# Optimization experiments

Measured on AMD Instinct MI355X. Metric: run time of the kernel, lower is better.

The kernel has to match this reference:

```python
import jax, jax.numpy as jnp
import numpy as np

# dims
B, TQ, NQ, DQ = 2, 32, 196, 896      # batch, chunks, queries/chunk, slow-feat dim
T, H, W, CIN = 32, 8, 8, 4           # fast feature video dims
EMB = 1024                           # fast input mapping (kv) dim
HID = 512                            # cross_attn_hidden_dim
NH = 4                               # heads
HD = HID // NH                       # head dim = 128
HALF = HD // 2                       # 64 rotary freq channels
SEC = [22, 21, 21]                   # 3D rope sections (t,h,w) over the 64 freqs
FF = 2 * HID
OUT = 896
BASE = 10000.0
QGRID = 14                           # 196 = 14x14 query spatial grid
EPS = 1e-5


def _p(key, shape, scale=0.02):
    return (jax.random.normal(key, shape, dtype=jnp.float32) * scale)


def setup_inputs() -> dict:
    key = jax.random.key(0)
    ks = jax.random.split(key, 20)
    inp = {
        "x": jax.random.normal(ks[0], (B, T, H, W, CIN), dtype=jnp.float32),
        "slow_feats": jax.random.normal(ks[1], (B, TQ, NQ, DQ), dtype=jnp.float32),
        "frame_num": jnp.full((B,), T, dtype=jnp.int32),
        # query_input_mapping: 896 -> 512
        "Wq_in": _p(ks[2], (DQ, HID)), "bq_in": jnp.zeros((HID,), jnp.float32),
        # fast input_mapping (linear): 4 -> 1024
        "Wm": _p(ks[3], (CIN, EMB)), "bm": jnp.zeros((EMB,), jnp.float32),
        # cross-attn projections
        "Wq": _p(ks[4], (HID, HID)), "bq": jnp.zeros((HID,), jnp.float32),
        "Wk": _p(ks[5], (EMB, HID)), "bk": jnp.zeros((HID,), jnp.float32),
        "Wv": _p(ks[6], (EMB, HID)), "bv": jnp.zeros((HID,), jnp.float32),
        "Wo": _p(ks[7], (HID, HID)), "bo": jnp.zeros((HID,), jnp.float32),
        # decoder layer norms + FFN (dim_feedforward = 2*hidden)
        "g1": jnp.ones((HID,), jnp.float32), "be1": jnp.zeros((HID,), jnp.float32),
        "W1": _p(ks[8], (HID, FF)), "b1": jnp.zeros((FF,), jnp.float32),
        "W2": _p(ks[9], (FF, HID)), "b2": jnp.zeros((HID,), jnp.float32),
        "g2": jnp.ones((HID,), jnp.float32), "be2": jnp.zeros((HID,), jnp.float32),
        # output MLP (mlp_depth=2): 512 -> 1024 -> GELU -> 896
        "M1": _p(ks[10], (HID, 2 * HID)), "bm1": jnp.zeros((2 * HID,), jnp.float32),
        "M2": _p(ks[11], (2 * HID, OUT)), "bm2": jnp.zeros((OUT,), jnp.float32),
    }
    return inp


def _ln(x, g, b):
    m = x.mean(-1, keepdims=True)
    v = jnp.var(x, axis=-1, keepdims=True)
    return (x - m) * jax.lax.rsqrt(v + EPS) * g + b


def _rope_cos_sin(pos):
    # pos: (N,3) float (t,h,w). Qwen2-style inv_freq over head_dim=128.
    inv_freq = 1.0 / (BASE ** (jnp.arange(0, HD, 2, dtype=jnp.float32) / HD))  # (64,)
    sel = jnp.asarray([0] * SEC[0] + [1] * SEC[1] + [2] * SEC[2])              # (64,)
    freqs = pos[:, sel] * inv_freq                                             # (N,64)
    emb = jnp.concatenate([freqs, freqs], axis=-1)                             # (N,128)
    return jnp.cos(emb), jnp.sin(emb)


def _rot_half(x):
    return jnp.concatenate([-x[..., HALF:], x[..., :HALF]], axis=-1)


def _positions():
    # query tokens: (chunk t, 14x14 grid)
    qt = jnp.repeat(jnp.arange(TQ), NQ)
    qg = jnp.tile(jnp.arange(NQ), TQ)
    q_pos = jnp.stack([qt, qg // QGRID, qg % QGRID], axis=-1).astype(jnp.float32)  # (6272,3)
    # kv tokens: (frame t, HxW grid)
    kt = jnp.repeat(jnp.arange(T), H * W)
    kg = jnp.tile(jnp.arange(H * W), T)
    k_pos = jnp.stack([kt, kg // W, kg % W], axis=-1).astype(jnp.float32)          # (2048,3)
    return q_pos, k_pos


def _forward(x, slow_feats, Wq_in, bq_in, Wm, bm, Wq, bq, Wk, bk, Wv, bv,
             Wo, bo, g1, be1, W1, b1, W2, b2, g2, be2, M1, bm1, M2, bm2):
    q_pos, k_pos = _positions()
    cos_q, sin_q = _rope_cos_sin(q_pos)   # (Nq,128)
    cos_k, sin_k = _rope_cos_sin(k_pos)   # (Nk,128)
    scale = 1.0 / jnp.sqrt(jnp.float32(HD))

    def per_sample(xi, si):
        # slow feats -> queries: (32,196,896) -> (6272,512)
        q_in = (si.reshape(TQ * NQ, DQ) @ Wq_in + bq_in)
        # fast feats -> kv tokens: (T,H,W,Cin) -> (2048,1024)
        kv = (xi.reshape(T * H * W, CIN) @ Wm + bm)
        # projections -> heads
        q = (q_in @ Wq + bq).reshape(-1, NH, HD)
        k = (kv @ Wk + bk).reshape(-1, NH, HD)
        v = (kv @ Wv + bv).reshape(-1, NH, HD)
        # 3D RoPE on q and k
        q = q * cos_q[:, None, :] + _rot_half(q) * sin_q[:, None, :]
        k = k * cos_k[:, None, :] + _rot_half(k) * sin_k[:, None, :]
        # cross attention
        attn = jnp.einsum('qhd,khd->hqk', q, k) * scale
        attn = jax.nn.softmax(attn, axis=-1)
        o = jnp.einsum('hqk,khd->qhd', attn, v).reshape(-1, HID)
        o = o @ Wo + bo
        # residual + norm + FFN + norm (post-norm decoder layer)
        h = _ln(q_in + o, g1, be1)
        ff = jax.nn.gelu(h @ W1 + b1) @ W2 + b2
        h = _ln(h + ff, g2, be2)
        # output MLP: Linear -> GELU -> Linear
        y = jax.nn.gelu(h @ M1 + bm1) @ M2 + bm2
        return y  # (6272, 896)

    return jax.vmap(per_sample)(x, slow_feats)  # (B, 6272, 896)


def reference(x, slow_feats, frame_num, Wq_in, bq_in, Wm, bm, Wq, bq, Wk, bk,
              Wv, bv, Wo, bo, g1, be1, W1, b1, W2, b2, g2, be2, M1, bm1, M2, bm2):
    # frame_num is the valid-frame count per sample; here all samples are full
    # length (frame_num == T), so no KV masking is needed.
    del frame_num
    return _forward(x, slow_feats, Wq_in, bq_in, Wm, bm, Wq, bq, Wk, bk, Wv, bv,
                    Wo, bo, g1, be1, W1, b1, W2, b2, g2, be2, M1, bm1, M2, bm2)
```

## Files before the change

kernel.cpp:

```cpp
#include <hip/hip_runtime.h>
#include <cstdint>
#include <cstddef>

#define BATCH 2
#define MQ 12544
#define ROWS_Q 6272
#define MK 4096
#define ROWS_K 2048
#define HID 512
#define NH 4
#define HD 128
#define EMB 1024
#define DQ 896
#define FF 1024
#define OUTD 896

typedef __bf16 bf16;
typedef unsigned int u32;
typedef bf16 bf16x8 __attribute__((ext_vector_type(8)));
typedef bf16 bf16x4 __attribute__((ext_vector_type(4)));
typedef float f32x4 __attribute__((ext_vector_type(4)));

enum { OP_BIAS = 0, OP_GELU = 1, OP_RES = 2 };

__device__ __forceinline__ float gelu_tanh(float x) {
    float x3 = x * x * x;
    return 0.5f * x * (1.0f + tanhf(0.7978845608028654f * (x + 0.044715f * x3)));
}

__device__ __forceinline__ void gld16(const bf16* g, bf16* l) {
    __builtin_amdgcn_global_load_lds(
        (const __attribute__((address_space(1))) unsigned int*)g,
        (__attribute__((address_space(3))) unsigned int*)l, 16, 0, 0);
}

__device__ __forceinline__ u32 pack_bf16(float a, float b) {
    union { bf16 h[2]; u32 w; } u;
    u.h[0] = (bf16)a; u.h[1] = (bf16)b;
    return u.w;
}

template <int OP, bool WF32, bool WB16>
__global__ __launch_bounds__(256) void mgemm(
    const bf16* __restrict__ A, const bf16* __restrict__ Bt,
    const float* __restrict__ bias, const float* __restrict__ res,
    float* __restrict__ Cf, bf16* __restrict__ Cb, int M, int N, int K)
{
    __shared__ __align__(16) bf16 As0[128 * 32];
    __shared__ __align__(16) bf16 As1[128 * 32];
    __shared__ __align__(16) bf16 Bs0[128 * 32];
    __shared__ __align__(16) bf16 Bs1[128 * 32];
    const int tid  = threadIdx.x;
    const int m0   = blockIdx.y * 128;
    const int n0   = blockIdx.x * 128;
    const int wave = tid >> 6, lane = tid & 63;
    const int wm = (wave >> 1) * 64, wn = (wave & 1) * 64;

    f32x4 acc[4][4] = {};

    const int srow = tid >> 2;
    const int scol = (tid & 3) * 8;
    const bf16* Ag = A  + (size_t)(m0 + srow) * K + scol;
    const bf16* Bg = Bt + (size_t)(n0 + srow) * K + scol;
    bf16* Al0 = &As0[tid * 8];
    bf16* Al1 = &As1[tid * 8];
    bf16* Bl0 = &Bs0[tid * 8];
    bf16* Bl1 = &Bs1[tid * 8];
    const size_t half = (size_t)64 * K;

    const int fr = lane & 15;
    const int kq = (lane >> 4) * 8;
    const bf16* pa0 = &As0[(wm + fr) * 32 + kq];
    const bf16* pa1 = &As1[(wm + fr) * 32 + kq];
    const bf16* pb0 = &Bs0[(wn + fr) * 32 + kq];
    const bf16* pb1 = &Bs1[(wn + fr) * 32 + kq];

    gld16(Ag,        Al0);
    gld16(Ag + half, Al0 + 64 * 32);
    gld16(Bg,        Bl0);
    gld16(Bg + half, Bl0 + 64 * 32);

    for (int k0 = 0; k0 < K; k0 += 64) {
        __syncthreads();
        gld16(Ag + k0 + 32,        Al1);
        gld16(Ag + k0 + 32 + half, Al1 + 64 * 32);
        gld16(Bg + k0 + 32,        Bl1);
        gld16(Bg + k0 + 32 + half, Bl1 + 64 * 32);
        {
            bf16x8 af[4], bfr[4];
            #pragma unroll
            for (int i = 0; i < 4; ++i) af[i]  = *(const bf16x8*)(pa0 + i * 16 * 32);
            #pragma unroll
            for (int j = 0; j < 4; ++j) bfr[j] = *(const bf16x8*)(pb0 + j * 16 * 32);
            #pragma unroll
            for (int i = 0; i < 4; ++i)
                #pragma unroll
                for (int j = 0; j < 4; ++j)
                    acc[i][j] = __builtin_amdgcn_mfma_f32_16x16x32_bf16(
                        af[i], bfr[j], acc[i][j], 0, 0, 0);
        }
        __syncthreads();
        if (k0 + 64 < K) {
            gld16(Ag + k0 + 64,        Al0);
            gld16(Ag + k0 + 64 + half, Al0 + 64 * 32);
            gld16(Bg + k0 + 64,        Bl0);
            gld16(Bg + k0 + 64 + half, Bl0 + 64 * 32);
        }
        {
            bf16x8 af[4], bfr[4];
            #pragma unroll
            for (int i = 0; i < 4; ++i) af[i]  = *(const bf16x8*)(pa1 + i * 16 * 32);
            #pragma unroll
            for (int j = 0; j < 4; ++j) bfr[j] = *(const bf16x8*)(pb1 + j * 16 * 32);
            #pragma unroll
            for (int i = 0; i < 4; ++i)
                #pragma unroll
                for (int j = 0; j < 4; ++j)
                    acc[i][j] = __builtin_amdgcn_mfma_f32_16x16x32_bf16(
                        af[i], bfr[j], acc[i][j], 0, 0, 0);
        }
    }

    const int colb = n0 + wn + (lane & 15);
    const int rowb = m0 + wm + (lane >> 4) * 4;
    #pragma unroll
    for (int i = 0; i < 4; ++i) {
        #pragma unroll
        for (int j = 0; j < 4; ++j) {
            const int c = colb + j * 16;
            const float bj = bias[c];
            #pragma unroll
            for (int r = 0; r < 4; ++r) {
                const int m = rowb + i * 16 + r;
                float v = acc[i][j][r] + bj;
                if (OP == OP_GELU) v = gelu_tanh(v);
                if (OP == OP_RES)  v += res[(size_t)m * N + c];
                if (WF32) Cf[(size_t)m * N + c] = v;
                if (WB16) Cb[(size_t)m * N + c] = (bf16)v;
            }
        }
    }
}

template <int OP, bool WF32, bool WB16>
__global__ __launch_bounds__(256) void mgemm64(
    const bf16* __restrict__ A, const bf16* __restrict__ Bt,
    const float* __restrict__ bias, const float* __restrict__ res,
    float* __restrict__ Cf, bf16* __restrict__ Cb, int M, int N, int K)
{
    __shared__ __align__(16) bf16 As0[64 * 32];
    __shared__ __align__(16) bf16 As1[64 * 32];
    __shared__ __align__(16) bf16 Bs0[128 * 32];
    __shared__ __align__(16) bf16 Bs1[128 * 32];
    const int tid  = threadIdx.x;
    const int m0   = blockIdx.y * 64;
    const int n0   = blockIdx.x * 128;
    const int wave = tid >> 6, lane = tid & 63;
    const int wm = (wave >> 1) * 32, wn = (wave & 1) * 64;

    f32x4 acc[2][4] = {};

    const int srow = tid >> 2;
    const int scol = (tid & 3) * 8;
    const bf16* Ag = A  + (size_t)(m0 + srow) * K + scol;
    const bf16* Bg = Bt + (size_t)(n0 + srow) * K + scol;
    bf16* Al0 = &As0[tid * 8];
    bf16* Al1 = &As1[tid * 8];
    bf16* Bl0 = &Bs0[tid * 8];
    bf16* Bl1 = &Bs1[tid * 8];
    const size_t half = (size_t)64 * K;

    const int fr = lane & 15;
    const int kq = (lane >> 4) * 8;
    const bf16* pa0 = &As0[(wm + fr) * 32 + kq];
    const bf16* pa1 = &As1[(wm + fr) * 32 + kq];
    const bf16* pb0 = &Bs0[(wn + fr) * 32 + kq];
    const bf16* pb1 = &Bs1[(wn + fr) * 32 + kq];

    gld16(Ag,        Al0);
    gld16(Bg,        Bl0);
    gld16(Bg + half, Bl0 + 64 * 32);

    for (int k0 = 0; k0 < K; k0 += 64) {
        __syncthreads();
        gld16(Ag + k0 + 32,        Al1);
        gld16(Bg + k0 + 32,        Bl1);
        gld16(Bg + k0 + 32 + half, Bl1 + 64 * 32);
        {
            bf16x8 af[2], bfr[4];
            #pragma unroll
            for (int i = 0; i < 2; ++i) af[i]  = *(const bf16x8*)(pa0 + i * 16 * 32);
            #pragma unroll
            for (int j = 0; j < 4; ++j) bfr[j] = *(const bf16x8*)(pb0 + j * 16 * 32);
            #pragma unroll
            for (int i = 0; i < 2; ++i)
                #pragma unroll
                for (int j = 0; j < 4; ++j)
                    acc[i][j] = __builtin_amdgcn_mfma_f32_16x16x32_bf16(
                        af[i], bfr[j], acc[i][j], 0, 0, 0);
        }
        __syncthreads();
        if (k0 + 64 < K) {
            gld16(Ag + k0 + 64,        Al0);
            gld16(Bg + k0 + 64,        Bl0);
            gld16(Bg + k0 + 64 + half, Bl0 + 64 * 32);
        }
        {
            bf16x8 af[2], bfr[4];
            #pragma unroll
            for (int i = 0; i < 2; ++i) af[i]  = *(const bf16x8*)(pa1 + i * 16 * 32);
            #pragma unroll
            for (int j = 0; j < 4; ++j) bfr[j] = *(const bf16x8*)(pb1 + j * 16 * 32);
            #pragma unroll
            for (int i = 0; i < 2; ++i)
                #pragma unroll
                for (int j = 0; j < 4; ++j)
                    acc[i][j] = __builtin_amdgcn_mfma_f32_16x16x32_bf16(
                        af[i], bfr[j], acc[i][j], 0, 0, 0);
        }
    }

    const int colb = n0 + wn + (lane & 15);
    const int rowb = m0 + wm + (lane >> 4) * 4;
    #pragma unroll
    for (int i = 0; i < 2; ++i) {
        #pragma unroll
        for (int j = 0; j < 4; ++j) {
            const int c = colb + j * 16;
            const float bj = bias[c];
            #pragma unroll
            for (int r = 0; r < 4; ++r) {
                const int m = rowb + i * 16 + r;
                float v = acc[i][j][r] + bj;
                if (OP == OP_GELU) v = gelu_tanh(v);
                if (OP == OP_RES)  v += res[(size_t)m * N + c];
                if (WF32) Cf[(size_t)m * N + c] = v;
                if (WB16) Cb[(size_t)m * N + c] = (bf16)v;
            }
        }
    }
}

struct TDesc { const float* src; bf16* dst; int K; int N; int tile0; };
struct TDescs { TDesc d[9]; };

__global__ __launch_bounds__(256) void transpose_all(TDescs td)
{
    __shared__ float t[32][33];
    const int blk = blockIdx.x;
    int i = 0;
    #pragma unroll
    for (int j = 1; j < 9; ++j) if (blk >= td.d[j].tile0) i = j;
    const float* src = td.d[i].src;
    bf16* dst = td.d[i].dst;
    const int K = td.d[i].K, N = td.d[i].N;
    const int local = blk - td.d[i].tile0;
    const int ntx = N >> 5;
    const int bx = local % ntx, by = local / ntx;
    const int x = threadIdx.x & 31, y = threadIdx.x >> 5;
    #pragma unroll
    for (int p = 0; p < 32; p += 8)
        t[y + p][x] = src[(size_t)(by * 32 + y + p) * N + bx * 32 + x];
    __syncthreads();
    #pragma unroll
    for (int p = 0; p < 32; p += 8)
        dst[(size_t)(bx * 32 + y + p) * K + by * 32 + x] = (bf16)t[x][y + p];
}

__global__ __launch_bounds__(256) void cvt_kernel(
    const float* __restrict__ in, bf16* __restrict__ out, int n4)
{
    int i = blockIdx.x * 256 + threadIdx.x;
    if (i >= n4) return;
    float4 v = ((const float4*)in)[i];
    out[4 * i + 0] = (bf16)v.x;
    out[4 * i + 1] = (bf16)v.y;
    out[4 * i + 2] = (bf16)v.z;
    out[4 * i + 3] = (bf16)v.w;
}

__global__ __launch_bounds__(256) void kv_kernel(
    const float* __restrict__ x, const float* __restrict__ Wm,
    const float* __restrict__ bm, bf16* __restrict__ kv)
{
    int idx = blockIdx.x * 256 + threadIdx.x;
    int r = idx >> 10, n = idx & 1023;
    float4 xv = *(const float4*)(x + (size_t)r * 4);
    float v = bm[n] + xv.x * Wm[n] + xv.y * Wm[1024 + n]
                    + xv.z * Wm[2048 + n] + xv.w * Wm[3072 + n];
    kv[idx] = (bf16)v;
}

__global__ __launch_bounds__(256) void rope_tab_kernel(float2* __restrict__ tab)
{
    int i = blockIdx.x * 256 + threadIdx.x;
    if (i >= 64 * 32) return;
    int f = i >> 5, pos = i & 31;
    float ang = (float)pos * exp2f(-(float)f * 0.20762050593045954f);
    tab[i] = make_float2(cosf(ang), sinf(ang));
}

__global__ __launch_bounds__(256) void rope_b_kernel(
    const bf16* __restrict__ in, bf16* __restrict__ out,
    const float2* __restrict__ tab,
    int tok, int gdiv, int wdiv, int total, float sc, int istr, int icoff)
{
    int idx = blockIdx.x * 256 + threadIdx.x;
    if (idx >= total) return;
    int row = idx >> 7;
    int r2 = idx & 127;
    int h = r2 >> 5;
    int j2 = r2 & 31;
    int j = 2 * j2;
    int n = row % tok;
    int t = n / gdiv;
    int g = n % gdiv;
    int gh = g / wdiv;
    int gw = g % wdiv;
    int j1 = j + 1;
    int pa_i = (j < 22)  ? t : (j < 43)  ? gh : gw;
    int pb_i = (j1 < 22) ? t : (j1 < 43) ? gh : gw;
    float2 ta = tab[j * 32 + pa_i];
    float2 tb = tab[j1 * 32 + pb_i];
    float ca = ta.x, sa = ta.y;
    float cb = tb.x, sb = tb.y;
    size_t ibase = (size_t)row * istr + icoff + (size_t)h * 128 + j;
    size_t obase = (size_t)row * 512 + (size_t)h * 128 + j;
    union { u32 w; bf16 e[2]; } ua, ub;
    ua.w = *(const u32*)(in + ibase);
    ub.w = *(const u32*)(in + ibase + 64);
    float x1a = (float)ua.e[0], x1b = (float)ua.e[1];
    float x2a = (float)ub.e[0], x2b = (float)ub.e[1];
    *(u32*)(out + obase)      = pack_bf16((x1a * ca - x2a * sa) * sc,
                                          (x1b * cb - x2b * sb) * sc);
    *(u32*)(out + obase + 64) = pack_bf16((x2a * ca + x1a * sa) * sc,
                                          (x2b * cb + x1b * sb) * sc);
}

__global__ __launch_bounds__(256) void vt_tiled(
    const bf16* __restrict__ kv16, bf16* __restrict__ vt)
{
    __shared__ bf16 t[64][72];
    const int tt = blockIdx.x * 64;
    const int d0 = blockIdx.y * 64;
    const int bh = blockIdx.z;
    const int b = bh >> 2, h = bh & 3;
    const int rr = threadIdx.x >> 4;
    const int cc = (threadIdx.x & 15) * 4;
    #pragma unroll
    for (int p = 0; p < 4; ++p) {
        int r = rr + p * 16;
        *(bf16x4*)&t[r][cc] = *(const bf16x4*)
            (kv16 + (size_t)(b * ROWS_K + tt + r) * 1024 + 512 + h * 128 + d0 + cc);
    }
    __syncthreads();
    #pragma unroll
    for (int p = 0; p < 4; ++p) {
        int r = rr + p * 16;
        bf16x4 v;
        v[0] = t[cc + 0][r]; v[1] = t[cc + 1][r];
        v[2] = t[cc + 2][r]; v[3] = t[cc + 3][r];
        *(bf16x4*)(vt + (size_t)bh * HD * ROWS_K + (size_t)(d0 + r) * ROWS_K + tt + cc) = v;
    }
}

__global__ __launch_bounds__(256) void ln_kernel(
    float* __restrict__ xb, const float* __restrict__ g,
    const float* __restrict__ be, bf16* __restrict__ out16)
{
    int wave = threadIdx.x >> 6, lane = threadIdx.x & 63;
    size_t row = (size_t)blockIdx.x * 4 + wave;
    float* xp = xb + row * 512;
    float4 a = ((const float4*)xp)[lane];
    float4 b = ((const float4*)xp)[lane + 64];
    float s  = a.x + a.y + a.z + a.w + b.x + b.y + b.z + b.w;
    float sq = a.x*a.x + a.y*a.y + a.z*a.z + a.w*a.w
             + b.x*b.x + b.y*b.y + b.z*b.z + b.w*b.w;
    #pragma unroll
    for (int off = 32; off; off >>= 1) {
        s  += __shfl_xor(s, off);
        sq += __shfl_xor(sq, off);
    }
    float mean = s * (1.0f / 512.0f);
    float var  = sq * (1.0f / 512.0f) - mean * mean;
    float rstd = rsqrtf(var + 1e-5f);
    float4 gv1 = ((const float4*)g)[lane],  gv2 = ((const float4*)g)[lane + 64];
    float4 bv1 = ((const float4*)be)[lane], bv2 = ((const float4*)be)[lane + 64];
    a.x = (a.x - mean) * rstd * gv1.x + bv1.x;
    a.y = (a.y - mean) * rstd * gv1.y + bv1.y;
    a.z = (a.z - mean) * rstd * gv1.z + bv1.z;
    a.w = (a.w - mean) * rstd * gv1.w + bv1.w;
    b.x = (b.x - mean) * rstd * gv2.x + bv2.x;
    b.y = (b.y - mean) * rstd * gv2.y + bv2.y;
    b.z = (b.z - mean) * rstd * gv2.z + bv2.z;
    b.w = (b.w - mean) * rstd * gv2.w + bv2.w;
    ((float4*)xp)[lane]      = a;
    ((float4*)xp)[lane + 64] = b;
    bf16* op = out16 + row * 512;
    *(u32*)(op + lane * 4)       = pack_bf16(a.x, a.y);
    *(u32*)(op + lane * 4 + 2)   = pack_bf16(a.z, a.w);
    *(u32*)(op + 256 + lane * 4)     = pack_bf16(b.x, b.y);
    *(u32*)(op + 256 + lane * 4 + 2) = pack_bf16(b.z, b.w);
}

__global__ __launch_bounds__(256, 2) void mattn_kernel(
    const bf16* __restrict__ qs, const bf16* __restrict__ ks,
    const bf16* __restrict__ vt, bf16* __restrict__ outb)
{
    __shared__ __align__(16) char smem[35840];
    bf16* Ksh = (bf16*)smem;
    bf16* Vsh = (bf16*)(smem + 17408);

    const int tid = threadIdx.x;
    const int wave = tid >> 6, lane = tid & 63;
    const int quad = lane >> 4, c = lane & 15;
    const int bid = blockIdx.x;
    const int bh = bid & 7;
    const int qt = bid >> 3;
    const int h  = bh & 3;
    const int b  = bh >> 2;

    const int q0 = qt * 128 + wave * 32;
    const bf16* qg = qs + (size_t)(b * ROWS_Q + q0) * HID + h * HD;
    const bf16* kg = ks + (size_t)(b * ROWS_K) * HID + h * HD;
    const bf16* vg = vt + (size_t)(b * NH + h) * HD * ROWS_K;

    bf16x8 qf[2][4];
    #pragma unroll
    for (int n = 0; n < 2; ++n)
        #pragma unroll
        for (int s = 0; s < 4; ++s)
            qf[n][s] = *(const bf16x8*)(qg + (size_t)(n * 16 + c) * HID + s * 32 + quad * 8);

    f32x4 o[8][2] = {};
    float m_i[2] = {-1e30f, -1e30f}, l_i[2] = {0.0f, 0.0f};

    const int st_t = tid >> 2;
    const int st_d = (tid & 3) * 32;
    const int sv_d = tid >> 1;
    const int sv_t = (tid & 1) * 32;

    for (int kt = 0; kt < 32; ++kt) {
        __syncthreads();
        {
            const bf16* src = kg + (size_t)(kt * 64 + st_t) * HID + st_d;
            bf16* dst = Ksh + st_t * 136 + st_d;
            #pragma unroll
            for (int i = 0; i < 4; ++i)
                *(bf16x8*)(dst + i * 8) = *(const bf16x8*)(src + i * 8);
        }
        {
            const bf16* src = vg + (size_t)sv_d * ROWS_K + kt * 64 + sv_t;
            bf16* dst = Vsh + sv_d * 72 + sv_t;
            #pragma unroll
            for (int i = 0; i < 4; ++i)
                *(bf16x8*)(dst + i * 8) = *(const bf16x8*)(src + i * 8);
        }
        __syncthreads();

        f32x4 s[4][2] = {};
        #pragma unroll
        for (int ksi = 0; ksi < 4; ++ksi) {
            bf16x8 kf[4];
            #pragma unroll
            for (int mi = 0; mi < 4; ++mi)
                kf[mi] = *(const bf16x8*)(Ksh + (mi * 16 + c) * 136 + ksi * 32 + quad * 8);
            #pragma unroll
            for (int mi = 0; mi < 4; ++mi)
                #pragma unroll
                for (int n = 0; n < 2; ++n)
                    s[mi][n] = __builtin_amdgcn_mfma_f32_16x16x32_bf16(
                        kf[mi], qf[n][ksi], s[mi][n], 0, 0, 0);
        }

        float alpha[2];
        #pragma unroll
        for (int n = 0; n < 2; ++n) {
            float mx = -1e30f;
            #pragma unroll
            for (int mi = 0; mi < 4; ++mi)
                #pragma unroll
                for (int r = 0; r < 4; ++r) mx = fmaxf(mx, s[mi][n][r]);
            mx = fmaxf(mx, __shfl_xor(mx, 16));
            mx = fmaxf(mx, __shfl_xor(mx, 32));
            float mn = fmaxf(m_i[n], mx);
            alpha[n] = __expf(m_i[n] - mn);
            m_i[n] = mn;
            float sm = 0.0f;
            #pragma unroll
            for (int mi = 0; mi < 4; ++mi)
                #pragma unroll
                for (int r = 0; r < 4; ++r) {
                    float p = __expf(s[mi][n][r] - mn);
                    s[mi][n][r] = p;
                    sm += p;
                }
            sm += __shfl_xor(sm, 16);
            sm += __shfl_xor(sm, 32);
            l_i[n] = l_i[n] * alpha[n] + sm;
            #pragma unroll
            for (int md = 0; md < 8; ++md) {
                o[md][n][0] *= alpha[n]; o[md][n][1] *= alpha[n];
                o[md][n][2] *= alpha[n]; o[md][n][3] *= alpha[n];
            }
        }

        u32 pk[4][2][2];
        #pragma unroll
        for (int mi = 0; mi < 4; ++mi)
            #pragma unroll
            for (int n = 0; n < 2; ++n) {
                pk[mi][n][0] = pack_bf16(s[mi][n][0], s[mi][n][1]);
                pk[mi][n][1] = pack_bf16(s[mi][n][2], s[mi][n][3]);
            }
        bf16x8 pf[2][2];
        #pragma unroll
        for (int kst = 0; kst < 2; ++kst)
            #pragma unroll
            for (int n = 0; n < 2; ++n) {
                union { bf16x8 v8; u32 d[4]; } u;
                #pragma unroll
                for (int dw = 0; dw < 4; ++dw) {
                    int srcl = ((quad & 1) * 2 + (dw >> 1)) * 16 + c;
                    u32 lo = (u32)__shfl((int)pk[2 * kst][n][dw & 1], srcl);
                    u32 hi = (u32)__shfl((int)pk[2 * kst + 1][n][dw & 1], srcl);
                    u.d[dw] = (quad >= 2) ? hi : lo;
                }
                pf[kst][n] = u.v8;
            }

        #pragma unroll
        for (int kst = 0; kst < 2; ++kst)
            #pragma unroll
            for (int md = 0; md < 8; ++md) {
                bf16x8 vf = *(const bf16x8*)(Vsh + (md * 16 + c) * 72 + kst * 32 + quad * 8);
                #pragma unroll
                for (int n = 0; n < 2; ++n)
                    o[md][n] = __builtin_amdgcn_mfma_f32_16x16x32_bf16(
                        vf, pf[kst][n], o[md][n], 0, 0, 0);
            }
    }

    __syncthreads();
    bf16* Osh = (bf16*)smem + wave * (32 * 136);
    float inv[2] = {1.0f / l_i[0], 1.0f / l_i[1]};
    #pragma unroll
    for (int md = 0; md < 8; ++md)
        #pragma unroll
        for (int n = 0; n < 2; ++n)
            #pragma unroll
            for (int hh = 0; hh < 2; ++hh) {
                u32 w = pack_bf16(o[md][n][2 * hh] * inv[n], o[md][n][2 * hh + 1] * inv[n]);
                int d = md * 16 + quad * 4 + 2 * hh;
                int qq = n * 16 + c;
                *(u32*)(Osh + qq * 136 + d) = w;
            }
    __syncthreads();
    bf16* og = outb + (size_t)(b * ROWS_Q + q0) * HID + h * HD;
    #pragma unroll
    for (int i = 0; i < 8; ++i) {
        int idx = i * 64 + lane;
        int qq = idx >> 4;
        int ch = idx & 15;
        bf16x8 vv = *(const bf16x8*)(Osh + qq * 136 + ch * 8);
        *(bf16x8*)(og + (size_t)qq * HID + ch * 8) = vv;
    }
}

extern "C" void kernel_launch(void* const* d_in, const int* in_sizes, int n_in,
                              void* d_out, int out_size, void* d_ws, size_t ws_size,
                              hipStream_t stream)
{
    const float* x     = (const float*)d_in[0];
    const float* slow  = (const float*)d_in[1];
    const float* Wq_in = (const float*)d_in[3];
    const float* bq_in = (const float*)d_in[4];
    const float* Wm    = (const float*)d_in[5];
    const float* bm    = (const float*)d_in[6];
    const float* Wq    = (const float*)d_in[7];
    const float* bq    = (const float*)d_in[8];
    const float* Wk    = (const float*)d_in[9];
    const float* bk    = (const float*)d_in[10];
    const float* Wv    = (const float*)d_in[11];
    const float* bv    = (const float*)d_in[12];
    const float* Wo    = (const float*)d_in[13];
    const float* bo    = (const float*)d_in[14];
    const float* g1    = (const float*)d_in[15];
    const float* be1   = (const float*)d_in[16];
    const float* W1    = (const float*)d_in[17];
    const float* b1    = (const float*)d_in[18];
    const float* W2    = (const float*)d_in[19];
    const float* b2    = (const float*)d_in[20];
    const float* g2    = (const float*)d_in[21];
    const float* be2   = (const float*)d_in[22];
    const float* M1    = (const float*)d_in[23];
    const float* bm1   = (const float*)d_in[24];
    const float* M2    = (const float*)d_in[25];
    const float* bm2   = (const float*)d_in[26];
    float* out = (float*)d_out;

    float* q_in_f = (float*)d_ws;
    float* ob     = q_in_f + (size_t)MQ * HID;
    float* bkv    = ob + (size_t)MQ * HID;
    bf16* shared_b = (bf16*)(bkv + 1024);
    bf16* q_in_b = shared_b + (size_t)MQ * FF;
    bf16* kv_b   = q_in_b + (size_t)MQ * HID;
    bf16* h_b    = kv_b + (size_t)MK * EMB;
    bf16* q16    = h_b + (size_t)MQ * HID;
    bf16* kv16   = q16 + (size_t)MQ * HID;
    bf16* qbt    = kv16 + (size_t)MK * EMB;
    bf16* kbt    = qbt + (size_t)MQ * HID;
    bf16* Vt     = kbt + (size_t)MK * HID;
    bf16* Wq_in_t = Vt + (size_t)8 * HD * ROWS_K;
    bf16* Wq_t  = Wq_in_t + 512 * 896;
    bf16* kvw_t = Wq_t + 512 * 512;
    bf16* Wo_t  = kvw_t + 1024 * 1024;
    bf16* W1_t  = Wo_t + 512 * 512;
    bf16* W2_t  = W1_t + 1024 * 512;
    bf16* M1_t  = W2_t + 512 * 1024;
    bf16* M2_t  = M1_t + 1024 * 512;
    bf16* slow_b = shared_b;
    bf16* attn_b = shared_b;
    bf16* ff1_b  = shared_b;
    bf16* m1_b   = shared_b;

    float2* rtab = (float2*)ob;

    dim3 blk(256);

    TDescs td;
    int t0 = 0;
    auto set = [&](int i, const float* s, bf16* d, int K, int N) {
        td.d[i] = {s, d, K, N, t0};
        t0 += (N / 32) * (K / 32);
    };
    set(0, Wq_in, Wq_in_t, 896, 512);
    set(1, Wq,    Wq_t,    512, 512);
    set(2, Wk,    kvw_t,              1024, 512);
    set(3, Wv,    kvw_t + 512 * 1024, 1024, 512);
    set(4, Wo,    Wo_t,    512, 512);
    set(5, W1,    W1_t,    512, 1024);
    set(6, W2,    W2_t,    1024, 512);
    set(7, M1,    M1_t,    512, 1024);
    set(8, M2,    M2_t,    1024, 896);
    transpose_all<<<t0, blk, 0, stream>>>(td);

    hipMemcpyAsync(bkv,       bk, 512 * sizeof(float), hipMemcpyDeviceToDevice, stream);
    hipMemcpyAsync(bkv + 512, bv, 512 * sizeof(float), hipMemcpyDeviceToDevice, stream);

    rope_tab_kernel<<<8, blk, 0, stream>>>(rtab);
    cvt_kernel<<<(MQ * DQ / 4 + 255) / 256, blk, 0, stream>>>(slow, slow_b, MQ * DQ / 4);
    kv_kernel<<<(MK * EMB) / 256, blk, 0, stream>>>(x, Wm, bm, kv_b);

    mgemm64<OP_BIAS, true, true><<<dim3(4, 196), blk, 0, stream>>>(
        slow_b, Wq_in_t, bq_in, nullptr, q_in_f, q_in_b, MQ, HID, DQ);
    mgemm64<OP_BIAS, false, true><<<dim3(4, 196), blk, 0, stream>>>(
        q_in_b, Wq_t, bq, nullptr, nullptr, q16, MQ, HID, HID);
    mgemm64<OP_BIAS, false, true><<<dim3(8, 64), blk, 0, stream>>>(
        kv_b, kvw_t, bkv, nullptr, nullptr, kv16, MK, 1024, EMB);
    rope_b_kernel<<<(MQ * 128 + 255) / 256, blk, 0, stream>>>(
        q16, qbt, rtab, ROWS_Q, 196, 14, MQ * 128, 0.08838834764831843f, 512, 0);
    rope_b_kernel<<<(MK * 128 + 255) / 256, blk, 0, stream>>>(
        kv16, kbt, rtab, ROWS_K, 64, 8, MK * 128, 1.0f, 1024, 0);
    vt_tiled<<<dim3(32, 2, 8), blk, 0, stream>>>(kv16, Vt);
    mattn_kernel<<<dim3(392), blk, 0, stream>>>(qbt, kbt, Vt, attn_b);
    mgemm64<OP_RES, true, false><<<dim3(4, 196), blk, 0, stream>>>(
        attn_b, Wo_t, bo, q_in_f, ob, nullptr, MQ, HID, HID);
    ln_kernel<<<MQ / 4, blk, 0, stream>>>(ob, g1, be1, h_b);
    mgemm<OP_GELU, false, true><<<dim3(8, 98), blk, 0, stream>>>(
        h_b, W1_t, b1, nullptr, nullptr, ff1_b, MQ, FF, HID);
    mgemm64<OP_RES, true, false><<<dim3(4, 196), blk, 0, stream>>>(
        ff1_b, W2_t, b2, ob, q_in_f, nullptr, MQ, HID, FF);
    ln_kernel<<<MQ / 4, blk, 0, stream>>>(q_in_f, g2, be2, h_b);
    mgemm<OP_GELU, false, true><<<dim3(8, 98), blk, 0, stream>>>(
        h_b, M1_t, bm1, nullptr, nullptr, m1_b, MQ, 2 * HID, HID);
    mgemm<OP_BIAS, true, false><<<dim3(7, 98), blk, 0, stream>>>(
        m1_b, M2_t, bm2, nullptr, out, nullptr, MQ, OUTD, 2 * HID);
}
```

Measured before the change: 565.8 us.

## Use 32x32 MFMA in 128-tile GEMM and merge small prep/rope kernels

```diff
diff --git a/kernel.cpp b/kernel.cpp
--- a/kernel.cpp
+++ b/kernel.cpp
@@ -20,6 +20,7 @@
 typedef bf16 bf16x8 __attribute__((ext_vector_type(8)));
 typedef bf16 bf16x4 __attribute__((ext_vector_type(4)));
 typedef float f32x4 __attribute__((ext_vector_type(4)));
+typedef float f32x16 __attribute__((ext_vector_type(16)));
 
 enum { OP_BIAS = 0, OP_GELU = 1, OP_RES = 2 };
 
@@ -56,7 +57,7 @@
     const int wave = tid >> 6, lane = tid & 63;
     const int wm = (wave >> 1) * 64, wn = (wave & 1) * 64;
 
-    f32x4 acc[4][4] = {};
+    f32x16 acc[2][2] = {};
 
     const int srow = tid >> 2;
     const int scol = (tid & 3) * 8;
@@ -68,12 +69,12 @@
     bf16* Bl1 = &Bs1[tid * 8];
     const size_t half = (size_t)64 * K;
 
-    const int fr = lane & 15;
-    const int kq = (lane >> 4) * 8;
-    const bf16* pa0 = &As0[(wm + fr) * 32 + kq];
-    const bf16* pa1 = &As1[(wm + fr) * 32 + kq];
-    const bf16* pb0 = &Bs0[(wn + fr) * 32 + kq];
-    const bf16* pb1 = &Bs1[(wn + fr) * 32 + kq];
+    const int r32 = lane & 31;
+    const int kh  = (lane >> 5) * 8;
+    const bf16* pa0 = &As0[(wm + r32) * 32 + kh];
+    const bf16* pa1 = &As1[(wm + r32) * 32 + kh];
+    const bf16* pb0 = &Bs0[(wn + r32) * 32 + kh];
+    const bf16* pb1 = &Bs1[(wn + r32) * 32 + kh];
 
     gld16(Ag,        Al0);
     gld16(Ag + half, Al0 + 64 * 32);
@@ -87,17 +88,22 @@
         gld16(Bg + k0 + 32,        Bl1);
         gld16(Bg + k0 + 32 + half, Bl1 + 64 * 32);
         {
-            bf16x8 af[4], bfr[4];
-            #pragma unroll
-            for (int i = 0; i < 4; ++i) af[i]  = *(const bf16x8*)(pa0 + i * 16 * 32);
-            #pragma unroll
-            for (int j = 0; j < 4; ++j) bfr[j] = *(const bf16x8*)(pb0 + j * 16 * 32);
-            #pragma unroll
-            for (int i = 0; i < 4; ++i)
-                #pragma unroll
-                for (int j = 0; j < 4; ++j)
-                    acc[i][j] = __builtin_amdgcn_mfma_f32_16x16x32_bf16(
-                        af[i], bfr[j], acc[i][j], 0, 0, 0);
+            bf16x8 af[2][2], bfr[2][2];
+            #pragma unroll
+            for (int ti = 0; ti < 2; ++ti)
+                #pragma unroll
+                for (int ks = 0; ks < 2; ++ks) {
+                    af[ti][ks]  = *(const bf16x8*)(pa0 + ti * 32 * 32 + ks * 16);
+                    bfr[ti][ks] = *(const bf16x8*)(pb0 + ti * 32 * 32 + ks * 16);
+                }
+            #pragma unroll
+            for (int ks = 0; ks < 2; ++ks)
+                #pragma unroll
+                for (int ti = 0; ti < 2; ++ti)
+                    #pragma unroll
+                    for (int tj = 0; tj < 2; ++tj)
+                        acc[ti][tj] = __builtin_amdgcn_mfma_f32_32x32x16_bf16(
+                            af[ti][ks], bfr[tj][ks], acc[ti][tj], 0, 0, 0);
         }
         __syncthreads();
         if (k0 + 64 < K) {
@@ -107,32 +113,37 @@
             gld16(Bg + k0 + 64 + half, Bl0 + 64 * 32);
         }
         {
-            bf16x8 af[4], bfr[4];
-            #pragma unroll
-            for (int i = 0; i < 4; ++i) af[i]  = *(const bf16x8*)(pa1 + i * 16 * 32);
-            #pragma unroll
-            for (int j = 0; j < 4; ++j) bfr[j] = *(const bf16x8*)(pb1 + j * 16 * 32);
-            #pragma unroll
-            for (int i = 0; i < 4; ++i)
-                #pragma unroll
-                for (int j = 0; j < 4; ++j)
-                    acc[i][j] = __builtin_amdgcn_mfma_f32_16x16x32_bf16(
-                        af[i], bfr[j], acc[i][j], 0, 0, 0);
-        }
-    }
-
-    const int colb = n0 + wn + (lane & 15);
-    const int rowb = m0 + wm + (lane >> 4) * 4;
-    #pragma unroll
-    for (int i = 0; i < 4; ++i) {
-        #pragma unroll
-        for (int j = 0; j < 4; ++j) {
-            const int c = colb + j * 16;
+            bf16x8 af[2][2], bfr[2][2];
+            #pragma unroll
+            for (int ti = 0; ti < 2; ++ti)
+                #pragma unroll
+                for (int ks = 0; ks < 2; ++ks) {
+                    af[ti][ks]  = *(const bf16x8*)(pa1 + ti * 32 * 32 + ks * 16);
+                    bfr[ti][ks] = *(const bf16x8*)(pb1 + ti * 32 * 32 + ks * 16);
+                }
+            #pragma unroll
+            for (int ks = 0; ks < 2; ++ks)
+                #pragma unroll
+                for (int ti = 0; ti < 2; ++ti)
+                    #pragma unroll
+                    for (int tj = 0; tj < 2; ++tj)
+                        acc[ti][tj] = __builtin_amdgcn_mfma_f32_32x32x16_bf16(
+                            af[ti][ks], bfr[tj][ks], acc[ti][tj], 0, 0, 0);
+        }
+    }
+
+    const int colb = n0 + wn + (lane & 31);
+    const int rowb = m0 + wm + (lane >> 5) * 4;
+    #pragma unroll
+    for (int ti = 0; ti < 2; ++ti) {
+        #pragma unroll
+        for (int tj = 0; tj < 2; ++tj) {
+            const int c = colb + tj * 32;
             const float bj = bias[c];
             #pragma unroll
-            for (int r = 0; r < 4; ++r) {
-                const int m = rowb + i * 16 + r;
-                float v = acc[i][j][r] + bj;
+            for (int r = 0; r < 16; ++r) {
+                const int m = rowb + ti * 32 + (r & 3) + (r >> 2) * 8;
+                float v = acc[ti][tj][r] + bj;
                 if (OP == OP_GELU) v = gelu_tanh(v);
                 if (OP == OP_RES)  v += res[(size_t)m * N + c];
                 if (WF32) Cf[(size_t)m * N + c] = v;
@@ -267,100 +278,111 @@
         dst[(size_t)(bx * 32 + y + p) * K + by * 32 + x] = (bf16)t[x][y + p];
 }
 
-__global__ __launch_bounds__(256) void cvt_kernel(
-    const float* __restrict__ in, bf16* __restrict__ out, int n4)
-{
-    int i = blockIdx.x * 256 + threadIdx.x;
-    if (i >= n4) return;
-    float4 v = ((const float4*)in)[i];
-    out[4 * i + 0] = (bf16)v.x;
-    out[4 * i + 1] = (bf16)v.y;
-    out[4 * i + 2] = (bf16)v.z;
-    out[4 * i + 3] = (bf16)v.w;
-}
-
-__global__ __launch_bounds__(256) void kv_kernel(
+#define PREP_NKV   16384
+#define PREP_NCVT  10976
+#define PREP_NTAB  8
+#define PREP_NBKV  4
+#define PREP_TOTAL (PREP_NKV + PREP_NCVT + PREP_NTAB + PREP_NBKV)
+
+__global__ __launch_bounds__(256) void prep_kernel(
     const float* __restrict__ x, const float* __restrict__ Wm,
-    const float* __restrict__ bm, bf16* __restrict__ kv)
-{
-    int idx = blockIdx.x * 256 + threadIdx.x;
-    int r = idx >> 10, n = idx & 1023;
-    float4 xv = *(const float4*)(x + (size_t)r * 4);
-    float v = bm[n] + xv.x * Wm[n] + xv.y * Wm[1024 + n]
-                    + xv.z * Wm[2048 + n] + xv.w * Wm[3072 + n];
-    kv[idx] = (bf16)v;
-}
-
-__global__ __launch_bounds__(256) void rope_tab_kernel(float2* __restrict__ tab)
-{
-    int i = blockIdx.x * 256 + threadIdx.x;
-    if (i >= 64 * 32) return;
-    int f = i >> 5, pos = i & 31;
-    float ang = (float)pos * exp2f(-(float)f * 0.20762050593045954f);
-    tab[i] = make_float2(cosf(ang), sinf(ang));
-}
-
-__global__ __launch_bounds__(256) void rope_b_kernel(
-    const bf16* __restrict__ in, bf16* __restrict__ out,
-    const float2* __restrict__ tab,
-    int tok, int gdiv, int wdiv, int total, float sc, int istr, int icoff)
-{
-    int idx = blockIdx.x * 256 + threadIdx.x;
-    if (idx >= total) return;
-    int row = idx >> 7;
-    int r2 = idx & 127;
-    int h = r2 >> 5;
-    int j2 = r2 & 31;
-    int j = 2 * j2;
-    int n = row % tok;
-    int t = n / gdiv;
-    int g = n % gdiv;
-    int gh = g / wdiv;
-    int gw = g % wdiv;
-    int j1 = j + 1;
-    int pa_i = (j < 22)  ? t : (j < 43)  ? gh : gw;
-    int pb_i = (j1 < 22) ? t : (j1 < 43) ? gh : gw;
-    float2 ta = tab[j * 32 + pa_i];
-    float2 tb = tab[j1 * 32 + pb_i];
-    float ca = ta.x, sa = ta.y;
-    float cb = tb.x, sb = tb.y;
-    size_t ibase = (size_t)row * istr + icoff + (size_t)h * 128 + j;
-    size_t obase = (size_t)row * 512 + (size_t)h * 128 + j;
-    union { u32 w; bf16 e[2]; } ua, ub;
-    ua.w = *(const u32*)(in + ibase);
-    ub.w = *(const u32*)(in + ibase + 64);
-    float x1a = (float)ua.e[0], x1b = (float)ua.e[1];
-    float x2a = (float)ub.e[0], x2b = (float)ub.e[1];
-    *(u32*)(out + obase)      = pack_bf16((x1a * ca - x2a * sa) * sc,
-                                          (x1b * cb - x2b * sb) * sc);
-    *(u32*)(out + obase + 64) = pack_bf16((x2a * ca + x1a * sa) * sc,
-                                          (x2b * cb + x1b * sb) * sc);
-}
-
-__global__ __launch_bounds__(256) void vt_tiled(
-    const bf16* __restrict__ kv16, bf16* __restrict__ vt)
+    const float* __restrict__ bm, bf16* __restrict__ kv,
+    const float* __restrict__ slow, bf16* __restrict__ slow_b,
+    const float* __restrict__ bk, const float* __restrict__ bv,
+    float* __restrict__ bkv, float2* __restrict__ tab)
+{
+    const int blk = blockIdx.x;
+    if (blk < PREP_NKV) {
+        int idx = blk * 256 + threadIdx.x;
+        int r = idx >> 10, n = idx & 1023;
+        float4 xv = *(const float4*)(x + (size_t)r * 4);
+        float v = bm[n] + xv.x * Wm[n] + xv.y * Wm[1024 + n]
+                        + xv.z * Wm[2048 + n] + xv.w * Wm[3072 + n];
+        kv[idx] = (bf16)v;
+    } else if (blk < PREP_NKV + PREP_NCVT) {
+        int i = (blk - PREP_NKV) * 256 + threadIdx.x;
+        float4 v = ((const float4*)slow)[i];
+        slow_b[4 * i + 0] = (bf16)v.x;
+        slow_b[4 * i + 1] = (bf16)v.y;
+        slow_b[4 * i + 2] = (bf16)v.z;
+        slow_b[4 * i + 3] = (bf16)v.w;
+    } else if (blk < PREP_NKV + PREP_NCVT + PREP_NTAB) {
+        int i = (blk - PREP_NKV - PREP_NCVT) * 256 + threadIdx.x;
+        int f = i >> 5, pos = i & 31;
+        float ang = (float)pos * exp2f(-(float)f * 0.20762050593045954f);
+        tab[i] = make_float2(cosf(ang), sinf(ang));
+    } else {
+        int i = (blk - PREP_NKV - PREP_NCVT - PREP_NTAB) * 256 + threadIdx.x;
+        bkv[i] = (i < 512) ? bk[i] : bv[i - 512];
+    }
+}
+
+__global__ __launch_bounds__(256) void rope_vt_kernel(
+    const bf16* __restrict__ q16, bf16* __restrict__ qbt,
+    const bf16* __restrict__ kv16, bf16* __restrict__ kbt,
+    const float2* __restrict__ tab, bf16* __restrict__ vt)
 {
     __shared__ bf16 t[64][72];
-    const int tt = blockIdx.x * 64;
-    const int d0 = blockIdx.y * 64;
-    const int bh = blockIdx.z;
-    const int b = bh >> 2, h = bh & 3;
-    const int rr = threadIdx.x >> 4;
-    const int cc = (threadIdx.x & 15) * 4;
-    #pragma unroll
-    for (int p = 0; p < 4; ++p) {
-        int r = rr + p * 16;
-        *(bf16x4*)&t[r][cc] = *(const bf16x4*)
-            (kv16 + (size_t)(b * ROWS_K + tt + r) * 1024 + 512 + h * 128 + d0 + cc);
-    }
-    __syncthreads();
-    #pragma unroll
-    for (int p = 0; p < 4; ++p) {
-        int r = rr + p * 16;
-        bf16x4 v;
-        v[0] = t[cc + 0][r]; v[1] = t[cc + 1][r];
-        v[2] = t[cc + 2][r]; v[3] = t[cc + 3][r];
-        *(bf16x4*)(vt + (size_t)bh * HD * ROWS_K + (size_t)(d0 + r) * ROWS_K + tt + cc) = v;
+    const int blk = blockIdx.x;
+    if (blk < 8320) {
+        const bool isq = blk < 6272;
+        const int idx = (isq ? blk : blk - 6272) * 256 + threadIdx.x;
+        const bf16* in = isq ? q16 : kv16;
+        bf16* out = isq ? qbt : kbt;
+        const int tok  = isq ? ROWS_Q : ROWS_K;
+        const int gdiv = isq ? 196 : 64;
+        const int wdiv = isq ? 14 : 8;
+        const float sc = isq ? 0.08838834764831843f : 1.0f;
+        const int istr = isq ? 512 : 1024;
+        int row = idx >> 7;
+        int r2 = idx & 127;
+        int h = r2 >> 5;
+        int j2 = r2 & 31;
+        int j = 2 * j2;
+        int n = row % tok;
+        int tt = n / gdiv;
+        int g = n % gdiv;
+        int gh = g / wdiv;
+        int gw = g % wdiv;
+        int j1 = j + 1;
+        int pa_i = (j < 22)  ? tt : (j < 43)  ? gh : gw;
+        int pb_i = (j1 < 22) ? tt : (j1 < 43) ? gh : gw;
+        float2 ta = tab[j * 32 + pa_i];
+        float2 tb = tab[j1 * 32 + pb_i];
+        size_t ibase = (size_t)row * istr + (size_t)h * 128 + j;
+        size_t obase = (size_t)row * 512 + (size_t)h * 128 + j;
+        union { u32 w; bf16 e[2]; } ua, ub;
+        ua.w = *(const u32*)(in + ibase);
+        ub.w = *(const u32*)(in + ibase + 64);
+        float x1a = (float)ua.e[0], x1b = (float)ua.e[1];
+        float x2a = (float)ub.e[0], x2b = (float)ub.e[1];
+        *(u32*)(out + obase)      = pack_bf16((x1a * ta.x - x2a * ta.y) * sc,
+                                              (x1b * tb.x - x2b * tb.y) * sc);
+        *(u32*)(out + obase + 64) = pack_bf16((x2a * ta.x + x1a * ta.y) * sc,
+                                              (x2b * tb.x + x1b * tb.y) * sc);
+    } else {
+        const int blk2 = blk - 8320;
+        const int tt = (blk2 & 31) * 64;
+        const int d0 = ((blk2 >> 5) & 1) * 64;
+        const int bh = blk2 >> 6;
+        const int b = bh >> 2, h = bh & 3;
+        const int rr = threadIdx.x >> 4;
+        const int cc = (threadIdx.x & 15) * 4;
+        #pragma unroll
+        for (int p = 0; p < 4; ++p) {
+            int r = rr + p * 16;
+            *(bf16x4*)&t[r][cc] = *(const bf16x4*)
+                (kv16 + (size_t)(b * ROWS_K + tt + r) * 1024 + 512 + h * 128 + d0 + cc);
+        }
+        __syncthreads();
+        #pragma unroll
+        for (int p = 0; p < 4; ++p) {
+            int r = rr + p * 16;
+            bf16x4 v;
+            v[0] = t[cc + 0][r]; v[1] = t[cc + 1][r];
+            v[2] = t[cc + 2][r]; v[3] = t[cc + 3][r];
+            *(bf16x4*)(vt + (size_t)bh * HD * ROWS_K + (size_t)(d0 + r) * ROWS_K + tt + cc) = v;
+        }
     }
 }
 
@@ -645,12 +667,8 @@
     set(8, M2,    M2_t,    1024, 896);
     transpose_all<<<t0, blk, 0, stream>>>(td);
 
-    hipMemcpyAsync(bkv,       bk, 512 * sizeof(float), hipMemcpyDeviceToDevice, stream);
-    hipMemcpyAsync(bkv + 512, bv, 512 * sizeof(float), hipMemcpyDeviceToDevice, stream);
-
-    rope_tab_kernel<<<8, blk, 0, stream>>>(rtab);
-    cvt_kernel<<<(MQ * DQ / 4 + 255) / 256, blk, 0, stream>>>(slow, slow_b, MQ * DQ / 4);
-    kv_kernel<<<(MK * EMB) / 256, blk, 0, stream>>>(x, Wm, bm, kv_b);
+    prep_kernel<<<PREP_TOTAL, blk, 0, stream>>>(
+        x, Wm, bm, kv_b, slow, slow_b, bk, bv, bkv, rtab);
 
     mgemm64<OP_BIAS, true, true><<<dim3(4, 196), blk, 0, stream>>>(
         slow_b, Wq_in_t, bq_in, nullptr, q_in_f, q_in_b, MQ, HID, DQ);
@@ -658,11 +676,7 @@
         q_in_b, Wq_t, bq, nullptr, nullptr, q16, MQ, HID, HID);
     mgemm64<OP_BIAS, false, true><<<dim3(8, 64), blk, 0, stream>>>(
         kv_b, kvw_t, bkv, nullptr, nullptr, kv16, MK, 1024, EMB);
-    rope_b_kernel<<<(MQ * 128 + 255) / 256, blk, 0, stream>>>(
-        q16, qbt, rtab, ROWS_Q, 196, 14, MQ * 128, 0.08838834764831843f, 512, 0);
-    rope_b_kernel<<<(MK * 128 + 255) / 256, blk, 0, stream>>>(
-        kv16, kbt, rtab, ROWS_K, 64, 8, MK * 128, 1.0f, 1024, 0);
-    vt_tiled<<<dim3(32, 2, 8), blk, 0, stream>>>(kv16, Vt);
+    rope_vt_kernel<<<dim3(8832), blk, 0, stream>>>(q16, qbt, kv16, kbt, rtab, Vt);
     mattn_kernel<<<dim3(392), blk, 0, stream>>>(qbt, kbt, Vt, attn_b);
     mgemm64<OP_RES, true, false><<<dim3(4, 196), blk, 0, stream>>>(
         attn_b, Wo_t, bo, q_in_f, ob, nullptr, MQ, HID, HID);
```

Result: faster. 553.2 us (-2.2%).
